# Optimization experiments

Measured on AMD Instinct MI355X. Metric: run time of the kernel, lower is better.

Reference implementation:

```python
import jax, jax.numpy as jnp
import numpy as np

B, J, PD = 4, 6890, 3
D, L, H, DH = 256, 4, 8, 64
INNER = H * DH          # 512
N = 2048                # downsample_dim (token count)
FF = 1024
M = 13780               # num_joints * upsample
HEAD_OUT = [3, 1, 3, 4, 3]  # mean3D, opacity, shs, rotations, scales


def setup_inputs() -> dict:
    ks = jax.random.split(jax.random.key(0), 16)
    rn = lambda k, shape, s=0.05: jax.random.normal(k, shape, jnp.float32) * s
    z = lambda shape: jnp.zeros(shape, jnp.float32)
    o = lambda shape: jnp.ones(shape, jnp.float32)
    return {
        'x': rn(ks[0], (B, J, PD), 1.0),
        'pre_emb_w': rn(ks[1], (PD, D)), 'pre_emb_b': z((D,)),
        'pre_conv_w': rn(ks[2], (N, J)), 'pre_conv_b': z((N,)),
        'pos_emb': rn(ks[3], (N, D), 0.02),
        'pre_norm_g': o((D,)), 'pre_norm_b': z((D,)),
        'ln1_g': o((L, D)), 'ln1_b': z((L, D)),
        'qkv_w': rn(ks[4], (L, D, 3 * INNER)),
        'out_w': rn(ks[5], (L, INNER, D)), 'out_b': z((L, D)),
        'ln2_g': o((L, D)), 'ln2_b': z((L, D)),
        'ff_w1': rn(ks[6], (L, D, FF)), 'ff_b1': z((L, FF)),
        'ff_w2': rn(ks[7], (L, FF, D)), 'ff_b2': z((L, D)),
        'up_w': rn(ks[8], (M, N)), 'up_b': z((M,)),
        'heads_w1': rn(ks[9], (5, D, D)), 'heads_b1': z((5, D)),
        'heads_w2': rn(ks[10], (5, D, 4)), 'heads_b2': z((5, 4)),
    }


def _ln(x, g, b, eps=1e-5):
    mu = jnp.mean(x, -1, keepdims=True)
    var = jnp.mean(jnp.square(x - mu), -1, keepdims=True)
    return (x - mu) * jax.lax.rsqrt(var + eps) * g + b


def _gelu(x):
    return jax.nn.gelu(x, approximate=False)  # torch nn.GELU default (erf)


def reference(x, pre_emb_w, pre_emb_b, pre_conv_w, pre_conv_b, pos_emb,
              pre_norm_g, pre_norm_b, ln1_g, ln1_b, qkv_w, out_w, out_b,
              ln2_g, ln2_b, ff_w1, ff_b1, ff_w2, ff_b2, up_w, up_b,
              heads_w1, heads_b1, heads_w2, heads_b2):
    scale = DH ** -0.5
    # token embedding: Linear(pose_dim->hidden) then Conv1d(num_joints->downsample_dim, k=1)
    h = x @ pre_emb_w + pre_emb_b                               # [B,J,D]
    h = jnp.einsum('bjd,nj->bnd', h, pre_conv_w) + pre_conv_b[None, :, None]  # [B,N,D]
    h = h + pos_emb[None]                                       # positional embedding
    h = _ln(h, pre_norm_g, pre_norm_b)
    # transformer encoder (pre-norm self-attn + FFN, residual)
    for i in range(L):
        y = _ln(h, ln1_g[i], ln1_b[i])
        qkv = y @ qkv_w[i]                                      # [B,N,3*INNER]
        q, k, v = jnp.split(qkv, 3, axis=-1)
        q = q.reshape(B, N, H, DH).transpose(0, 2, 1, 3)        # [B,H,N,DH]
        k = k.reshape(B, N, H, DH).transpose(0, 2, 1, 3)
        v = v.reshape(B, N, H, DH).transpose(0, 2, 1, 3)
        dots = jnp.einsum('bhnd,bhmd->bhnm', q, k) * scale      # [B,H,N,N]
        attn = jax.nn.softmax(dots, axis=-1)
        o = jnp.einsum('bhnm,bhmd->bhnd', attn, v)
        o = o.transpose(0, 2, 1, 3).reshape(B, N, INNER)
        h = o @ out_w[i] + out_b[i] + h
        y = _ln(h, ln2_g[i], ln2_b[i])
        h = _gelu(y @ ff_w1[i] + ff_b1[i]) @ ff_w2[i] + ff_b2[i] + h
    # upsample conv: Conv1d(downsample_dim -> num_joints*upsample, k=1)
    u = jnp.einsum('bnd,mn->bmd', h, up_w) + up_b[None, :, None]  # [B,M,D]
    # 5 gaussian-attribute heads (stacked; out dims padded to 4 and sliced)
    hid = _gelu(jnp.einsum('bmd,kde->kbme', u, heads_w1) + heads_b1[:, None, None, :])
    op = jnp.einsum('kbme,keo->kbmo', hid, heads_w2) + heads_b2[:, None, None, :]
    outs = [op[i, ..., :HEAD_OUT[i]] for i in range(5)]
    return jnp.concatenate(outs, axis=-1)                       # [B,M,14]
```

## Files before the change

### kernel.cpp

```cpp
#include <hip/hip_runtime.h>
#include <math.h>

#define B_ 4
#define J_ 6890
#define D_ 256
#define L_ 4
#define H_ 8
#define DH_ 64
#define INNER_ 512
#define N_ 2048
#define FF_ 1024
#define M_ 13780
#define MP_ 13824

typedef float4 f4;
typedef __attribute__((ext_vector_type(8))) short s16x8;
typedef __attribute__((ext_vector_type(4))) float fx4;

__device__ __forceinline__ float b2f(short s) {
    return __uint_as_float(((unsigned int)(unsigned short)s) << 16);
}
__device__ __forceinline__ short f2bf(float f) {
    unsigned int u = __float_as_uint(f);
    unsigned int r = (u + 0x7FFFu + ((u >> 16) & 1u)) >> 16;
    return (short)r;
}
__device__ __forceinline__ float gelu_f(float v) {
    return 0.5f * v * (1.0f + erff(v * 0.70710678118654752440f));
}

__global__ __launch_bounds__(256) void embed_ln_kernel(
    const float* __restrict__ x, const float* __restrict__ emb_w,
    const float* __restrict__ emb_b, const float* __restrict__ conv_w,
    const float* __restrict__ conv_b, const float* __restrict__ pos_emb,
    const float* __restrict__ g, const float* __restrict__ beta,
    float* __restrict__ hout)
{
    const int n = blockIdx.x, b = blockIdx.y, t = threadIdx.x;
    const float* wrow = conv_w + (size_t)n * J_;
    const float* xb = x + (size_t)b * J_ * 3;
    float t0 = 0.f, t1 = 0.f, t2 = 0.f, s = 0.f;
    for (int j = t; j < J_; j += 256) {
        float w = wrow[j];
        s  += w;
        t0 += w * xb[3*j+0];
        t1 += w * xb[3*j+1];
        t2 += w * xb[3*j+2];
    }
    __shared__ float red[16];
    #pragma unroll
    for (int off = 32; off > 0; off >>= 1) {
        t0 += __shfl_down(t0, off, 64);
        t1 += __shfl_down(t1, off, 64);
        t2 += __shfl_down(t2, off, 64);
        s  += __shfl_down(s,  off, 64);
    }
    const int lane = t & 63, wid = t >> 6;
    if (lane == 0) { red[wid*4+0]=t0; red[wid*4+1]=t1; red[wid*4+2]=t2; red[wid*4+3]=s; }
    __syncthreads();
    t0 = red[0]+red[4]+red[8]+red[12];
    t1 = red[1]+red[5]+red[9]+red[13];
    t2 = red[2]+red[6]+red[10]+red[14];
    s  = red[3]+red[7]+red[11]+red[15];
    __syncthreads();

    float val = t0*emb_w[t] + t1*emb_w[D_+t] + t2*emb_w[2*D_+t]
              + s*emb_b[t] + conv_b[n] + pos_emb[(size_t)n*D_ + t];

    float sv = val, sq = val*val;
    #pragma unroll
    for (int off = 32; off > 0; off >>= 1) {
        sv += __shfl_down(sv, off, 64);
        sq += __shfl_down(sq, off, 64);
    }
    if (lane == 0) { red[wid*2]=sv; red[wid*2+1]=sq; }
    __syncthreads();
    sv = red[0]+red[2]+red[4]+red[6];
    sq = red[1]+red[3]+red[5]+red[7];
    float mu   = sv * (1.f/D_);
    float var  = sq * (1.f/D_) - mu*mu;
    float rstd = rsqrtf(fmaxf(var, 0.f) + 1e-5f);
    hout[((size_t)(b*N_ + n))*D_ + t] = (val - mu)*rstd*g[t] + beta[t];
}

__global__ __launch_bounds__(256) void ln_bf_kernel(
    const float* __restrict__ in, short* __restrict__ outp,
    const float* __restrict__ g, const float* __restrict__ beta)
{
    const int row = blockIdx.x, t = threadIdx.x;
    float v = in[(size_t)row*D_ + t];
    float sv = v, sq = v*v;
    #pragma unroll
    for (int off = 32; off > 0; off >>= 1) {
        sv += __shfl_down(sv, off, 64);
        sq += __shfl_down(sq, off, 64);
    }
    __shared__ float red[8];
    const int lane = t & 63, wid = t >> 6;
    if (lane == 0) { red[wid*2]=sv; red[wid*2+1]=sq; }
    __syncthreads();
    sv = red[0]+red[2]+red[4]+red[6];
    sq = red[1]+red[3]+red[5]+red[7];
    float mu   = sv * (1.f/D_);
    float var  = sq * (1.f/D_) - mu*mu;
    float rstd = rsqrtf(fmaxf(var, 0.f) + 1e-5f);
    outp[(size_t)row*D_ + t] = f2bf((v - mu)*rstd*g[t] + beta[t]);
}

__global__ __launch_bounds__(256) void tcvt_kernel(
    const float* __restrict__ in, short* __restrict__ outp,
    int R, int C, long inZ, long outZ)
{
    in   += (size_t)blockIdx.z * inZ;
    outp += (size_t)blockIdx.z * outZ;
    __shared__ float tile[32][33];
    const int c0 = blockIdx.x * 32, r0 = blockIdx.y * 32;
    const int t = threadIdx.x;
    const int row = t >> 3, c4 = (t & 7) * 4;
    f4 v = *(const f4*)&in[(size_t)(r0 + row)*C + c0 + c4];
    tile[row][c4+0] = v.x; tile[row][c4+1] = v.y;
    tile[row][c4+2] = v.z; tile[row][c4+3] = v.w;
    __syncthreads();
    const int oc = t >> 3, r4 = (t & 7) * 4;
    short* dst = &outp[(size_t)(c0 + oc)*R + r0 + r4];
    #pragma unroll
    for (int j = 0; j < 4; j++) dst[j] = f2bf(tile[r4 + j][oc]);
}

__global__ __launch_bounds__(256) void cvt_kernel(
    const float* __restrict__ in, short* __restrict__ outp)
{
    const size_t i = ((size_t)blockIdx.x * 256 + threadIdx.x) * 8;
    f4 a = *(const f4*)&in[i];
    f4 b = *(const f4*)&in[i + 4];
    s16x8 s;
    s[0]=f2bf(a.x); s[1]=f2bf(a.y); s[2]=f2bf(a.z); s[3]=f2bf(a.w);
    s[4]=f2bf(b.x); s[5]=f2bf(b.y); s[6]=f2bf(b.z); s[7]=f2bf(b.w);
    *(s16x8*)&outp[i] = s;
}

template<int BIAS_COL, int BIAS_ROW, int GELU, int RESID, int OUT_BF16>
__global__ __launch_bounds__(256) void gemm_bf16_kernel(
    const short* __restrict__ A, int lda, long sA,
    const short* __restrict__ Bt, int ldb, long sB,
    void* __restrict__ Cv, int ldc, long sC,
    const float* __restrict__ bias, long sBias,
    int M, int K)
{
    const int z = blockIdx.z;
    A  += (size_t)z * sA;
    Bt += (size_t)z * sB;
    const int m0 = blockIdx.y * 128, n0 = blockIdx.x * 128;
    const int t = threadIdx.x;
    const int lane = t & 63, w = t >> 6;
    const int wm = w >> 1, wn = w & 1;

    __shared__ short As[128*32];
    __shared__ short Bs[128*32];

    fx4 acc[4][4];
    #pragma unroll
    for (int i = 0; i < 4; i++)
        #pragma unroll
        for (int j = 0; j < 4; j++)
            acc[i][j] = (fx4){0.f, 0.f, 0.f, 0.f};

    const int r_a = t >> 2, co_a = (t & 3) * 8;
    const int fr = lane & 15, fg = (lane >> 4) * 8;

    for (int k0 = 0; k0 < K; k0 += 32) {
        s16x8 va0 = *(const s16x8*)&A [(size_t)(m0 + r_a)      * lda + k0 + co_a];
        s16x8 va1 = *(const s16x8*)&A [(size_t)(m0 + 64 + r_a) * lda + k0 + co_a];
        s16x8 vb0 = *(const s16x8*)&Bt[(size_t)(n0 + r_a)      * ldb + k0 + co_a];
        s16x8 vb1 = *(const s16x8*)&Bt[(size_t)(n0 + 64 + r_a) * ldb + k0 + co_a];
        __syncthreads();
        *(s16x8*)&As[r_a*32 + co_a]          = va0;
        *(s16x8*)&As[(64 + r_a)*32 + co_a]   = va1;
        *(s16x8*)&Bs[r_a*32 + co_a]          = vb0;
        *(s16x8*)&Bs[(64 + r_a)*32 + co_a]   = vb1;
        __syncthreads();

        s16x8 af[4], bfr[4];
        #pragma unroll
        for (int i = 0; i < 4; i++) {
            af[i]  = *(const s16x8*)&As[(wm*64 + i*16 + fr)*32 + fg];
            bfr[i] = *(const s16x8*)&Bs[(wn*64 + i*16 + fr)*32 + fg];
        }
        #pragma unroll
        for (int i = 0; i < 4; i++)
            #pragma unroll
            for (int j = 0; j < 4; j++)
                acc[i][j] = __builtin_amdgcn_mfma_f32_16x16x32_bf16(
                                af[i], bfr[j], acc[i][j], 0, 0, 0);
    }

    const int cr = (lane >> 4) * 4, cc = lane & 15;
    #pragma unroll
    for (int i = 0; i < 4; i++) {
        #pragma unroll
        for (int j = 0; j < 4; j++) {
            const int gcol = n0 + wn*64 + j*16 + cc;
            #pragma unroll
            for (int r = 0; r < 4; r++) {
                const int grow = m0 + wm*64 + i*16 + cr + r;
                if (grow >= M) continue;
                float v = acc[i][j][r];
                if (BIAS_COL) v += bias[(size_t)z*sBias + gcol];
                if (BIAS_ROW) v += bias[(size_t)z*sBias + grow];
                if (GELU)     v = gelu_f(v);
                if (OUT_BF16) {
                    short* C = (short*)Cv + (size_t)z*sC;
                    C[(size_t)grow*ldc + gcol] = f2bf(v);
                } else {
                    float* C = (float*)Cv + (size_t)z*sC;
                    float* cp = &C[(size_t)grow*ldc + gcol];
                    float o = v;
                    if (RESID) o += *cp;
                    *cp = o;
                }
            }
        }
    }
}

__global__ __launch_bounds__(256) void attn_mfma_kernel(
    const short* __restrict__ qkv,
    short* __restrict__ o)
{
    const int q0 = blockIdx.x * 128;
    const int head = blockIdx.y;
    const int b = blockIdx.z;
    const int t = threadIdx.x;
    const int lane = t & 63, wq = t >> 6;
    const int g = lane >> 4, i16 = lane & 15;

    __shared__ short Kl[64*64];
    __shared__ short Vtl[64*64];
    __shared__ short Pl[128*64];
    char* const Kb = (char*)Kl;
    char* const Vb = (char*)Vtl;
    char* const Pb = (char*)Pl;

    s16x8 qreg[2][2];
    #pragma unroll
    for (int qf = 0; qf < 2; qf++) {
        const int qg = q0 + wq*32 + i16 + 16*qf;
        const short* qp = qkv + (size_t)(b*N_ + qg)*1536 + head*DH_;
        #pragma unroll
        for (int ks = 0; ks < 2; ks++)
            qreg[qf][ks] = *(const s16x8*)&qp[8*g + 32*ks];
    }

    fx4 oacc[4][2];
    #pragma unroll
    for (int df = 0; df < 4; df++)
        #pragma unroll
        for (int qf = 0; qf < 2; qf++)
            oacc[df][qf] = (fx4){0.f, 0.f, 0.f, 0.f};
    float mst[2] = {-INFINITY, -INFINITY};
    float lst[2] = {0.f, 0.f};

    const int sr = t >> 2, scol = (t & 3) * 16;
    const int swr = (sr & 7) << 4;
    const int qrow0 = wq*32 + i16, qrow1 = qrow0 + 16;
    const int swq0 = (qrow0 & 7) << 4, swq1 = (qrow1 & 7) << 4;

    for (int kt = 0; kt < N_/64; ++kt) {
        const short* kp = qkv + (size_t)(b*N_ + kt*64 + sr)*1536 + INNER_ + head*DH_ + scol;
        s16x8 k0 = *(const s16x8*)kp;
        s16x8 k1 = *(const s16x8*)(kp + 8);
        s16x8 v0 = *(const s16x8*)(kp + INNER_);
        s16x8 v1 = *(const s16x8*)(kp + INNER_ + 8);
        __syncthreads();
        *(s16x8*)(Kb + sr*128 + ((2*scol)      ^ swr)) = k0;
        *(s16x8*)(Kb + sr*128 + ((2*scol + 16) ^ swr)) = k1;
        #pragma unroll
        for (int j = 0; j < 8; j++) {
            *(short*)(Vb + (scol+j)*128   + ((2*sr) ^ (j<<4))) = v0[j];
            *(short*)(Vb + (scol+8+j)*128 + ((2*sr) ^ (j<<4))) = v1[j];
        }
        __syncthreads();

        fx4 sacc[4][2];
        #pragma unroll
        for (int kvf = 0; kvf < 4; kvf++)
            #pragma unroll
            for (int qf = 0; qf < 2; qf++)
                sacc[kvf][qf] = (fx4){0.f, 0.f, 0.f, 0.f};
        #pragma unroll
        for (int ks = 0; ks < 2; ks++) {
            #pragma unroll
            for (int kvf = 0; kvf < 4; kvf++) {
                const int kv = i16 + 16*kvf;
                s16x8 ka = *(const s16x8*)(Kb + kv*128 + ((16*g + 64*ks) ^ ((kv&7)<<4)));
                #pragma unroll
                for (int qf = 0; qf < 2; qf++)
                    sacc[kvf][qf] = __builtin_amdgcn_mfma_f32_16x16x32_bf16(
                                        ka, qreg[qf][ks], sacc[kvf][qf], 0, 0, 0);
            }
        }

        #pragma unroll
        for (int qf = 0; qf < 2; qf++) {
            float sv[16];
            #pragma unroll
            for (int kvf = 0; kvf < 4; kvf++)
                #pragma unroll
                for (int r = 0; r < 4; r++)
                    sv[kvf*4+r] = sacc[kvf][qf][r] * 0.125f;
            float tm = sv[0];
            #pragma unroll
            for (int k = 1; k < 16; k++) tm = fmaxf(tm, sv[k]);
            tm = fmaxf(tm, __shfl_xor(tm, 16, 64));
            tm = fmaxf(tm, __shfl_xor(tm, 32, 64));
            const float mn  = fmaxf(qf ? mst[1] : mst[0], tm);
            const float scl = __expf((qf ? mst[1] : mst[0]) - mn);
            float rs = 0.f;
            float p[16];
            #pragma unroll
            for (int k = 0; k < 16; k++) { p[k] = __expf(sv[k] - mn); rs += p[k]; }
            rs += __shfl_xor(rs, 16, 64);
            rs += __shfl_xor(rs, 32, 64);
            if (qf) { lst[1] = lst[1]*scl + rs; mst[1] = mn; }
            else    { lst[0] = lst[0]*scl + rs; mst[0] = mn; }
            #pragma unroll
            for (int df = 0; df < 4; df++) {
                oacc[df][qf][0] *= scl; oacc[df][qf][1] *= scl;
                oacc[df][qf][2] *= scl; oacc[df][qf][3] *= scl;
            }
            const int qr = qf ? qrow1 : qrow0;
            const int sq = qf ? swq1 : swq0;
            #pragma unroll
            for (int kvf = 0; kvf < 4; kvf++) {
                uint2 wv;
                wv.x = (unsigned int)(unsigned short)f2bf(p[4*kvf+0]) |
                       ((unsigned int)(unsigned short)f2bf(p[4*kvf+1]) << 16);
                wv.y = (unsigned int)(unsigned short)f2bf(p[4*kvf+2]) |
                       ((unsigned int)(unsigned short)f2bf(p[4*kvf+3]) << 16);
                *(uint2*)(Pb + qr*128 + ((8*g + 32*kvf) ^ sq)) = wv;
            }
        }

        asm volatile("s_waitcnt lgkmcnt(0)" ::: "memory");
        __builtin_amdgcn_sched_barrier(0);

        #pragma unroll
        for (int ks = 0; ks < 2; ks++) {
            s16x8 pf0 = *(const s16x8*)(Pb + qrow0*128 + ((16*g + 64*ks) ^ swq0));
            s16x8 pf1 = *(const s16x8*)(Pb + qrow1*128 + ((16*g + 64*ks) ^ swq1));
            #pragma unroll
            for (int df = 0; df < 4; df++) {
                const int dh = i16 + 16*df;
                s16x8 va = *(const s16x8*)(Vb + dh*128 + ((16*g + 64*ks) ^ ((dh&7)<<4)));
                oacc[df][0] = __builtin_amdgcn_mfma_f32_16x16x32_bf16(va, pf0, oacc[df][0], 0, 0, 0);
                oacc[df][1] = __builtin_amdgcn_mfma_f32_16x16x32_bf16(va, pf1, oacc[df][1], 0, 0, 0);
            }
        }
    }

    const float inv0 = 1.f / lst[0], inv1 = 1.f / lst[1];
    #pragma unroll
    for (int df = 0; df < 4; df++)
        #pragma unroll
        for (int r = 0; r < 4; r++) {
            const int dh = 4*g + r + 16*df;
            *(short*)(Pb + qrow0*128 + ((2*dh) ^ swq0)) = f2bf(oacc[df][0][r]*inv0);
            *(short*)(Pb + qrow1*128 + ((2*dh) ^ swq1)) = f2bf(oacc[df][1][r]*inv1);
        }
    __syncthreads();
    {
        const int qr = t >> 1, h2 = t & 1;
        const int sq = (qr & 7) << 4;
        short* op = o + (size_t)(b*N_ + q0 + qr)*INNER_ + head*DH_ + 32*h2;
        #pragma unroll
        for (int e = 0; e < 4; e++) {
            s16x8 vv = *(const s16x8*)(Pb + qr*128 + ((64*h2 + 16*e) ^ sq));
            *(s16x8*)&op[8*e] = vv;
        }
    }
}

__global__ __launch_bounds__(256) void heads2_kernel(
    const short* __restrict__ hid, const float* __restrict__ w2k,
    const float* __restrict__ b2k, float* __restrict__ outp,
    int koff, int kcnt)
{
    const int t = threadIdx.x, z = blockIdx.y;
    __shared__ float w2s[1024];
    *(f4*)&w2s[t*4] = *(const f4*)&w2k[t*4];
    __syncthreads();

    const int m = blockIdx.x*64 + (t >> 2);
    const int q = t & 3;
    float a0 = 0.f, a1 = 0.f, a2 = 0.f, a3 = 0.f;
    if (m < M_) {
        const s16x8* hp = (const s16x8*)(hid + ((size_t)z*MP_ + m)*D_ + q*64);
        #pragma unroll
        for (int c8 = 0; c8 < 8; c8++) {
            s16x8 v = hp[c8];
            #pragma unroll
            for (int j = 0; j < 8; j++) {
                float f = b2f(v[j]);
                const float* wv = &w2s[(q*64 + c8*8 + j)*4];
                a0 += f*wv[0]; a1 += f*wv[1]; a2 += f*wv[2]; a3 += f*wv[3];
            }
        }
    }
    a0 += __shfl_xor(a0, 1, 64); a0 += __shfl_xor(a0, 2, 64);
    a1 += __shfl_xor(a1, 1, 64); a1 += __shfl_xor(a1, 2, 64);
    a2 += __shfl_xor(a2, 1, 64); a2 += __shfl_xor(a2, 2, 64);
    a3 += __shfl_xor(a3, 1, 64); a3 += __shfl_xor(a3, 2, 64);
    if (q == 0 && m < M_) {
        float av[4] = {a0, a1, a2, a3};
        for (int o2 = 0; o2 < kcnt; o2++)
            outp[((size_t)z*M_ + m)*14 + koff + o2] = av[o2] + b2k[o2];
    }
}

extern "C" void kernel_launch(void* const* d_in, const int* in_sizes, int n_in,
                              void* d_out, int out_size, void* d_ws, size_t ws_size,
                              hipStream_t stream)
{
    const float* x          = (const float*)d_in[0];
    const float* pre_emb_w  = (const float*)d_in[1];
    const float* pre_emb_b  = (const float*)d_in[2];
    const float* pre_conv_w = (const float*)d_in[3];
    const float* pre_conv_b = (const float*)d_in[4];
    const float* pos_emb    = (const float*)d_in[5];
    const float* pre_norm_g = (const float*)d_in[6];
    const float* pre_norm_b = (const float*)d_in[7];
    const float* ln1_g      = (const float*)d_in[8];
    const float* ln1_b      = (const float*)d_in[9];
    const float* qkv_w      = (const float*)d_in[10];
    const float* out_w      = (const float*)d_in[11];
    const float* out_b      = (const float*)d_in[12];
    const float* ln2_g      = (const float*)d_in[13];
    const float* ln2_b      = (const float*)d_in[14];
    const float* ff_w1      = (const float*)d_in[15];
    const float* ff_b1      = (const float*)d_in[16];
    const float* ff_w2      = (const float*)d_in[17];
    const float* ff_b2      = (const float*)d_in[18];
    const float* up_w       = (const float*)d_in[19];
    const float* up_b       = (const float*)d_in[20];
    const float* heads_w1   = (const float*)d_in[21];
    const float* heads_b1   = (const float*)d_in[22];
    const float* heads_w2   = (const float*)d_in[23];
    const float* heads_b2   = (const float*)d_in[24];
    float* out = (float*)d_out;

    char* ws = (char*)d_ws;
    float* h      = (float*)(ws);
    char*  R2     = ws + 8388608;
    short* y_bf   = (short*)(R2);
    short* qkv_bf = (short*)(R2 + 4194304);
    short* ffmid  = qkv_bf;
    short* obuf   = (short*)(R2 + 29360128);
    short* qkvT   = (short*)(R2 + 37748736);
    short* outT   = (short*)(R2 + 40894464);
    short* ff1T   = (short*)(R2 + 41943040);
    short* ff2T   = (short*)(R2 + 44040192);
    short* upw_bf = (short*)(R2);
    short* hT     = (short*)(ws + 65011712);
    short* u_bf   = (short*)(ws + 69206016);
    short* w1T    = (short*)(ws + 97517568);
    short* hid    = (short*)(ws + 98172928);

    tcvt_kernel<<<dim3(1536/32,  256/32, 4), 256, 0, stream>>>(qkv_w,    qkvT, 256, 1536, 256L*1536, 1536L*256);
    tcvt_kernel<<<dim3( 256/32,  512/32, 4), 256, 0, stream>>>(out_w,    outT, 512,  256, 512L*256,  256L*512);
    tcvt_kernel<<<dim3(1024/32,  256/32, 4), 256, 0, stream>>>(ff_w1,    ff1T, 256, 1024, 256L*1024, 1024L*256);
    tcvt_kernel<<<dim3( 256/32, 1024/32, 4), 256, 0, stream>>>(ff_w2,    ff2T, 1024, 256, 1024L*256, 256L*1024);
    tcvt_kernel<<<dim3( 256/32,  256/32, 5), 256, 0, stream>>>(heads_w1, w1T,  256,  256, 256L*256,  256L*256);

    embed_ln_kernel<<<dim3(N_, B_), 256, 0, stream>>>(
        x, pre_emb_w, pre_emb_b, pre_conv_w, pre_conv_b, pos_emb,
        pre_norm_g, pre_norm_b, h);

    const int rows = B_ * N_;
    for (int i = 0; i < L_; i++) {
        ln_bf_kernel<<<rows, 256, 0, stream>>>(h, y_bf, ln1_g + i*D_, ln1_b + i*D_);
        gemm_bf16_kernel<0,0,0,0,1><<<dim3(12, rows/128, 1), 256, 0, stream>>>(
            y_bf, 256, 0, qkvT + (size_t)i*1536*256, 256, 0,
            qkv_bf, 1536, 0, nullptr, 0, rows, 256);
        attn_mfma_kernel<<<dim3(N_/128, H_, B_), 256, 0, stream>>>(qkv_bf, obuf);
        gemm_bf16_kernel<1,0,0,1,0><<<dim3(2, rows/128, 1), 256, 0, stream>>>(
            obuf, 512, 0, outT + (size_t)i*256*512, 512, 0,
            h, 256, 0, out_b + i*D_, 0, rows, 512);
        ln_bf_kernel<<<rows, 256, 0, stream>>>(h, y_bf, ln2_g + i*D_, ln2_b + i*D_);
        gemm_bf16_kernel<1,0,1,0,1><<<dim3(8, rows/128, 1), 256, 0, stream>>>(
            y_bf, 256, 0, ff1T + (size_t)i*1024*256, 256, 0,
            ffmid, 1024, 0, ff_b1 + i*FF_, 0, rows, 256);
        gemm_bf16_kernel<1,0,0,1,0><<<dim3(2, rows/128, 1), 256, 0, stream>>>(
            ffmid, 1024, 0, ff2T + (size_t)i*256*1024, 1024, 0,
            h, 256, 0, ff_b2 + i*D_, 0, rows, 1024);
    }

    cvt_kernel<<<13780, 256, 0, stream>>>(up_w, upw_bf);
    tcvt_kernel<<<dim3(256/32, 2048/32, 4), 256, 0, stream>>>(h, hT, 2048, 256, 2048L*256, 256L*2048);
    gemm_bf16_kernel<0,1,0,0,1><<<dim3(2, MP_/128, 4), 256, 0, stream>>>(
        upw_bf, 2048, 0, hT, 2048, 256L*2048,
        u_bf, 256, (long)MP_*256, up_b, 0, M_, 2048);

    static const int koff_h[5] = {0, 3, 4, 7, 11};
    static const int kcnt_h[5] = {3, 1, 3, 4, 3};
    for (int k = 0; k < 5; k++) {
        gemm_bf16_kernel<1,0,1,0,1><<<dim3(2, MP_/128, 4), 256, 0, stream>>>(
            u_bf, 256, (long)MP_*256, w1T + (size_t)k*256*256, 256, 0,
            hid, 256, (long)MP_*256, heads_b1 + k*256, 0, M_, 256);
        heads2_kernel<<<dim3(MP_/64, 4), 256, 0, stream>>>(
            hid, heads_w2 + (size_t)k*256*4, heads_b2 + k*4, out, koff_h[k], kcnt_h[k]);
    }
}
```

Measured before the change: 1.602 ms.

## Fuse attribute heads into one kernel and use direct global-to-LDS loads

Replaces the five per-head GEMM plus projection launch pairs with a single fused kernel. It computes the hidden layer with MFMA, applies bias and GELU, and reduces against the small second-layer weights in registers and LDS, so the bf16 hidden tensor never goes to global memory. The upsample GEMM is batched into one launch by treating the four batches as one wider N dimension. GEMM tile staging now uses global_load_lds instead of register round trips. The cost is more register pressure and a larger LDS footprint in the fused kernel.

```diff
diff --git a/kernel.cpp b/kernel.cpp
--- a/kernel.cpp
+++ b/kernel.cpp
@@ -29,6 +29,12 @@
     return 0.5f * v * (1.0f + erff(v * 0.70710678118654752440f));
 }
 
+__device__ __forceinline__ void gld16(void* lds, const void* g) {
+    __builtin_amdgcn_global_load_lds(
+        (const __attribute__((address_space(1))) void*)g,
+        (__attribute__((address_space(3))) void*)lds, 16, 0, 0);
+}
+
 __global__ __launch_bounds__(256) void embed_ln_kernel(
     const float* __restrict__ x, const float* __restrict__ emb_w,
     const float* __restrict__ emb_b, const float* __restrict__ conv_w,
@@ -165,19 +171,17 @@
         for (int j = 0; j < 4; j++)
             acc[i][j] = (fx4){0.f, 0.f, 0.f, 0.f};
 
-    const int r_a = t >> 2, co_a = (t & 3) * 8;
+    const int srow = lane >> 2, scol = (lane & 3) * 8;
     const int fr = lane & 15, fg = (lane >> 4) * 8;
 
     for (int k0 = 0; k0 < K; k0 += 32) {
-        s16x8 va0 = *(const s16x8*)&A [(size_t)(m0 + r_a)      * lda + k0 + co_a];
-        s16x8 va1 = *(const s16x8*)&A [(size_t)(m0 + 64 + r_a) * lda + k0 + co_a];
-        s16x8 vb0 = *(const s16x8*)&Bt[(size_t)(n0 + r_a)      * ldb + k0 + co_a];
-        s16x8 vb1 = *(const s16x8*)&Bt[(size_t)(n0 + 64 + r_a) * ldb + k0 + co_a];
         __syncthreads();
-        *(s16x8*)&As[r_a*32 + co_a]          = va0;
-        *(s16x8*)&As[(64 + r_a)*32 + co_a]   = va1;
-        *(s16x8*)&Bs[r_a*32 + co_a]          = vb0;
-        *(s16x8*)&Bs[(64 + r_a)*32 + co_a]   = vb1;
+        #pragma unroll
+        for (int c = 0; c < 2; c++) {
+            const int r = w*16 + c*64;
+            gld16(&As[r*32], &A [(size_t)(m0 + r + srow)*lda + k0 + scol]);
+            gld16(&Bs[r*32], &Bt[(size_t)(n0 + r + srow)*ldb + k0 + scol]);
+        }
         __syncthreads();
 
         s16x8 af[4], bfr[4];
@@ -380,40 +384,125 @@
     }
 }
 
-__global__ __launch_bounds__(256) void heads2_kernel(
-    const short* __restrict__ hid, const float* __restrict__ w2k,
-    const float* __restrict__ b2k, float* __restrict__ outp,
-    int koff, int kcnt)
-{
-    const int t = threadIdx.x, z = blockIdx.y;
+__global__ __launch_bounds__(512) void heads_fused_kernel(
+    const short* __restrict__ u,
+    const short* __restrict__ w1T,
+    const float* __restrict__ b1,
+    const float* __restrict__ w2,
+    const float* __restrict__ b2,
+    float* __restrict__ outp)
+{
+    const int m0 = blockIdx.x * 128;
+    const int b  = blockIdx.y;
+    const int k  = blockIdx.z;
+    const int t  = threadIdx.x;
+    const int lane = t & 63, w = t >> 6;
+    const int wm = w >> 2, wn = w & 3;
+
+    __shared__ short As[128*32];
+    __shared__ short Bs[256*32];
     __shared__ float w2s[1024];
-    *(f4*)&w2s[t*4] = *(const f4*)&w2k[t*4];
-    __syncthreads();
-
-    const int m = blockIdx.x*64 + (t >> 2);
-    const int q = t & 3;
-    float a0 = 0.f, a1 = 0.f, a2 = 0.f, a3 = 0.f;
-    if (m < M_) {
-        const s16x8* hp = (const s16x8*)(hid + ((size_t)z*MP_ + m)*D_ + q*64);
-        #pragma unroll
-        for (int c8 = 0; c8 < 8; c8++) {
-            s16x8 v = hp[c8];
-            #pragma unroll
-            for (int j = 0; j < 8; j++) {
-                float f = b2f(v[j]);
-                const float* wv = &w2s[(q*64 + c8*8 + j)*4];
-                a0 += f*wv[0]; a1 += f*wv[1]; a2 += f*wv[2]; a3 += f*wv[3];
-            }
-        }
-    }
-    a0 += __shfl_xor(a0, 1, 64); a0 += __shfl_xor(a0, 2, 64);
-    a1 += __shfl_xor(a1, 1, 64); a1 += __shfl_xor(a1, 2, 64);
-    a2 += __shfl_xor(a2, 1, 64); a2 += __shfl_xor(a2, 2, 64);
-    a3 += __shfl_xor(a3, 1, 64); a3 += __shfl_xor(a3, 2, 64);
-    if (q == 0 && m < M_) {
-        float av[4] = {a0, a1, a2, a3};
-        for (int o2 = 0; o2 < kcnt; o2++)
-            outp[((size_t)z*M_ + m)*14 + koff + o2] = av[o2] + b2k[o2];
+    __shared__ float b1s[256];
+    __shared__ float red4[4][128][4];
+
+    if (t < 256) b1s[t] = b1[k*256 + t];
+    w2s[t]       = w2[k*1024 + t];
+    w2s[t + 512] = w2[k*1024 + t + 512];
+
+    fx4 acc[4][4];
+    #pragma unroll
+    for (int i = 0; i < 4; i++)
+        #pragma unroll
+        for (int j = 0; j < 4; j++)
+            acc[i][j] = (fx4){0.f, 0.f, 0.f, 0.f};
+
+    const short* Ab = u + (size_t)b * 256;
+    const short* Bb = w1T + (size_t)k * 65536;
+    const int srow = lane >> 2, scol = (lane & 3) * 8;
+    const int fr = lane & 15, fg = (lane >> 4) * 8;
+
+    for (int k0 = 0; k0 < 256; k0 += 32) {
+        __syncthreads();
+        {
+            const int r = w*16;
+            gld16(&As[r*32], &Ab[(size_t)(m0 + r + srow)*1024 + k0 + scol]);
+            gld16(&Bs[r*32],         &Bb[(size_t)(r + srow)*256 + k0 + scol]);
+            gld16(&Bs[(128+r)*32],   &Bb[(size_t)(128 + r + srow)*256 + k0 + scol]);
+        }
+        __syncthreads();
+
+        s16x8 af[4], bfr[4];
+        #pragma unroll
+        for (int i = 0; i < 4; i++) {
+            af[i]  = *(const s16x8*)&As[(wm*64 + i*16 + fr)*32 + fg];
+            bfr[i] = *(const s16x8*)&Bs[(wn*64 + i*16 + fr)*32 + fg];
+        }
+        #pragma unroll
+        for (int i = 0; i < 4; i++)
+            #pragma unroll
+            for (int j = 0; j < 4; j++)
+                acc[i][j] = __builtin_amdgcn_mfma_f32_16x16x32_bf16(
+                                af[i], bfr[j], acc[i][j], 0, 0, 0);
+    }
+
+    const int cr = (lane >> 4) * 4, cc = lane & 15;
+    float p[4][4][4];
+    #pragma unroll
+    for (int i = 0; i < 4; i++)
+        #pragma unroll
+        for (int r = 0; r < 4; r++)
+            #pragma unroll
+            for (int o = 0; o < 4; o++) p[i][r][o] = 0.f;
+
+    #pragma unroll
+    for (int i = 0; i < 4; i++) {
+        #pragma unroll
+        for (int j = 0; j < 4; j++) {
+            const int col = wn*64 + j*16 + cc;
+            const float bb = b1s[col];
+            const float* wv = &w2s[col*4];
+            #pragma unroll
+            for (int r = 0; r < 4; r++) {
+                const float hv = gelu_f(acc[i][j][r] + bb);
+                #pragma unroll
+                for (int o = 0; o < 4; o++) p[i][r][o] += hv * wv[o];
+            }
+        }
+    }
+    #pragma unroll
+    for (int i = 0; i < 4; i++)
+        #pragma unroll
+        for (int r = 0; r < 4; r++)
+            #pragma unroll
+            for (int o = 0; o < 4; o++) {
+                float v = p[i][r][o];
+                v += __shfl_xor(v, 1, 64);
+                v += __shfl_xor(v, 2, 64);
+                v += __shfl_xor(v, 4, 64);
+                v += __shfl_xor(v, 8, 64);
+                p[i][r][o] = v;
+            }
+    if (cc == 0) {
+        #pragma unroll
+        for (int i = 0; i < 4; i++)
+            #pragma unroll
+            for (int r = 0; r < 4; r++)
+                #pragma unroll
+                for (int o = 0; o < 4; o++)
+                    red4[wn][wm*64 + i*16 + cr + r][o] = p[i][r][o];
+    }
+    __syncthreads();
+
+    const int koff = (k==0) ? 0 : (k==1) ? 3 : (k==2) ? 4 : (k==3) ? 7 : 11;
+    const int kcnt = (k==1) ? 1 : (k==3) ? 4 : 3;
+    {
+        const int row = t >> 2, o = t & 3;
+        const int m = m0 + row;
+        if (o < kcnt && m < M_) {
+            float v = red4[0][row][o] + red4[1][row][o]
+                    + red4[2][row][o] + red4[3][row][o] + b2[k*4 + o];
+            outp[((size_t)b*M_ + m)*14 + koff + o] = v;
+        }
     }
 }
 
@@ -463,7 +552,6 @@
     short* hT     = (short*)(ws + 65011712);
     short* u_bf   = (short*)(ws + 69206016);
     short* w1T    = (short*)(ws + 97517568);
-    short* hid    = (short*)(ws + 98172928);
 
     tcvt_kernel<<<dim3(1536/32,  256/32, 4), 256, 0, stream>>>(qkv_w,    qkvT, 256, 1536, 256L*1536, 1536L*256);
     tcvt_kernel<<<dim3( 256/32,  512/32, 4), 256, 0, stream>>>(out_w,    outT, 512,  256, 512L*256,  256L*512);
@@ -496,17 +584,10 @@
 
     cvt_kernel<<<13780, 256, 0, stream>>>(up_w, upw_bf);
     tcvt_kernel<<<dim3(256/32, 2048/32, 4), 256, 0, stream>>>(h, hT, 2048, 256, 2048L*256, 256L*2048);
-    gemm_bf16_kernel<0,1,0,0,1><<<dim3(2, MP_/128, 4), 256, 0, stream>>>(
-        upw_bf, 2048, 0, hT, 2048, 256L*2048,
-        u_bf, 256, (long)MP_*256, up_b, 0, M_, 2048);
-
-    static const int koff_h[5] = {0, 3, 4, 7, 11};
-    static const int kcnt_h[5] = {3, 1, 3, 4, 3};
-    for (int k = 0; k < 5; k++) {
-        gemm_bf16_kernel<1,0,1,0,1><<<dim3(2, MP_/128, 4), 256, 0, stream>>>(
-            u_bf, 256, (long)MP_*256, w1T + (size_t)k*256*256, 256, 0,
-            hid, 256, (long)MP_*256, heads_b1 + k*256, 0, M_, 256);
-        heads2_kernel<<<dim3(MP_/64, 4), 256, 0, stream>>>(
-            hid, heads_w2 + (size_t)k*256*4, heads_b2 + k*4, out, koff_h[k], kcnt_h[k]);
-    }
-}
+    gemm_bf16_kernel<0,1,0,0,1><<<dim3(8, MP_/128, 1), 256, 0, stream>>>(
+        upw_bf, 2048, 0, hT, 2048, 0,
+        u_bf, 1024, 0, up_b, 0, M_, 2048);
+
+    heads_fused_kernel<<<dim3(MP_/128, B_, 5), 512, 0, stream>>>(
+        u_bf, w1T, heads_b1, heads_w2, heads_b2, out);
+}
```

After: 1.605 ms. No clear change (+0.2%).
